# Kernel tuning notes

Hardware: AMD Instinct MI355X
Metric: run time of the kernel (lower is better)

## Reference

```python
import jax, jax.numpy as jnp
import numpy as np

B, C, L, H = 4, 128, 4096, 4
GROUPS, EPS = 32, 1e-5


def group_norm(x, gamma, beta):
    # x: [B, C, L]; normalize per (batch, group) over (C//G, L)
    b, c, l = x.shape
    xg = x.reshape(b, GROUPS, c // GROUPS, l)
    mu = jnp.mean(xg, axis=(2, 3), keepdims=True)
    var = jnp.var(xg, axis=(2, 3), keepdims=True)
    xn = ((xg - mu) * jax.lax.rsqrt(var + EPS)).reshape(b, c, l)
    return xn * gamma[None, :, None] + beta[None, :, None]


def setup_inputs() -> dict:
    key = jax.random.key(0)
    k1, k2, k3 = jax.random.split(key, 3)
    return {
        "x": jax.random.normal(k1, (B, C, L), dtype=jnp.float32),
        "w_qkv": jax.random.normal(k2, (3 * C, C), dtype=jnp.float32) * 0.02,
        "w_proj": jax.random.normal(k3, (C, C), dtype=jnp.float32) * 0.02,
        "b_proj": jnp.zeros((C,), dtype=jnp.float32),
        "gn_gamma": jnp.ones((C,), dtype=jnp.float32),
        "gn_beta": jnp.zeros((C,), dtype=jnp.float32),
    }


def reference(x, w_qkv, w_proj, b_proj, gn_gamma, gn_beta):
    b, c, l = x.shape
    hd = c // H
    h = group_norm(x, gn_gamma, gn_beta)
    # 1x1 conv == channel matmul: [B, 3C, L]
    qkv = jnp.einsum('oc,bcl->bol', w_qkv, h)
    # torch reshape(B*H, 3C/H, L).chunk(3, dim=1): per-head contiguous slices
    qkv = qkv.reshape(b, H, 3 * hd, l)
    q, k, v = qkv[:, :, :hd], qkv[:, :, hd:2 * hd], qkv[:, :, 2 * hd:]
    scale = 1.0 / np.sqrt(np.sqrt(hd)).astype(np.float32)
    attn = jnp.einsum('bhct,bhcs->bhts', q * scale, k * scale)
    attn = jax.nn.softmax(attn, axis=-1)
    o = jnp.einsum('bhts,bhcs->bhct', attn, v).reshape(b, c, l)
    o = jnp.einsum('oc,bcl->bol', w_proj, o) + b_proj[None, :, None]
    return o + x
```

## Files before the change

### kernel.cpp

```cpp
#include <hip/hip_runtime.h>
#include <hip/hip_bf16.h>
#include <cstdint>
#include <cstddef>


#define B_ 4
#define C_ 128
#define L_ 4096
#define H_ 4
#define HD_ 32
#define NG_ 32
#define CPG_ 4
#define EPS_ 1e-5f
#define QKSCALE_ 0.5050097650430367f

typedef __attribute__((ext_vector_type(8))) short bf16x8;
typedef __attribute__((ext_vector_type(8))) unsigned short u16x8;
typedef __attribute__((ext_vector_type(4))) float f32x4;
typedef __attribute__((ext_vector_type(2))) _Float16 f16x2;
typedef __attribute__((ext_vector_type(4))) _Float16 f16x4;

#if __has_builtin(__builtin_amdgcn_exp2f)
#define EXP2F(x) __builtin_amdgcn_exp2f(x)
#else
#define EXP2F(x) exp2f(x)
#endif

#if __has_builtin(__builtin_amdgcn_mfma_f32_16x16x16f16)
#define MFMA_PV(a, b, c) __builtin_amdgcn_mfma_f32_16x16x16f16((a), (b), (c), 0, 0, 0)
#elif __has_builtin(__builtin_amdgcn_mfma_f32_16x16x16_f16)
#define MFMA_PV(a, b, c) __builtin_amdgcn_mfma_f32_16x16x16_f16((a), (b), (c), 0, 0, 0)
#else
#define MFMA_PV(a, b, c) __builtin_amdgcn_mfma_f32_16x16x16f16((a), (b), (c), 0, 0, 0)
#endif

__device__ __forceinline__ float bu2f(unsigned short u) {
  return __builtin_bit_cast(float, (unsigned int)(((unsigned int)u) << 16));
}
__device__ __forceinline__ unsigned short f2bu(float f) {
  unsigned int u = __builtin_bit_cast(unsigned int, f);
  unsigned int r = (u + 0x7fffu + ((u >> 16) & 1u)) >> 16;
  return (unsigned short)r;
}
__device__ __forceinline__ float4 u42f4(ushort4 u) {
  return make_float4(bu2f(u.x), bu2f(u.y), bu2f(u.z), bu2f(u.w));
}
__device__ __forceinline__ unsigned int pkbf(float a, float b) {
  return (unsigned int)f2bu(a) | ((unsigned int)f2bu(b) << 16);
}
__device__ __forceinline__ f16x2 pkhf2(float a, float b) {
#if __has_builtin(__builtin_amdgcn_cvt_pkrtz)
  return __builtin_bit_cast(f16x2, __builtin_amdgcn_cvt_pkrtz(a, b));
#else
  f16x2 r;
  r[0] = (_Float16)a;
  r[1] = (_Float16)b;
  return r;
#endif
}
__device__ __forceinline__ unsigned int pkhf(float a, float b) {
  return __builtin_bit_cast(unsigned int, pkhf2(a, b));
}

__device__ __forceinline__ bool detect_fast(const ushort* x) {
  __shared__ int flag_s;
  int t = threadIdx.x;
  if (t < 64) {
    int e = (x[t] >> 7) & 0xFF;
    unsigned long long m = __ballot((e < 64) || (e > 192));
    if (t == 0) flag_s = (__popcll(m) > 4) ? 1 : 0;
  }
  __syncthreads();
  return flag_s != 0;
}

__device__ __forceinline__ float4 ldx4(const void* x, size_t idx, bool f32) {
  if (f32) return *((const float4*)x + (idx >> 2));
  ushort4 u = *((const ushort4*)x + (idx >> 2));
  return u42f4(u);
}

__global__ __launch_bounds__(512) void gn_fused(const void* __restrict__ x,
                                                const void* __restrict__ wq,
                                                const void* __restrict__ wp,
                                                const void* __restrict__ bp,
                                                const void* __restrict__ gm,
                                                const void* __restrict__ bt,
                                                ushort* __restrict__ wq_b,
                                                ushort* __restrict__ wp_b,
                                                float* __restrict__ bp_f,
                                                ushort* __restrict__ h_bf) {
  bool f32 = detect_fast((const ushort*)x);
  int blk = blockIdx.x;
  int t = threadIdx.x;

  if (blk >= 128) {
    int i0 = ((blk - 128) * 512 + t) * 4;
#pragma unroll
    for (int k = 0; k < 4; ++k) {
      int i = i0 + k;
      if (i >= 65664) break;
      if (i < 49152) {
        wq_b[i] = f32 ? f2bu(((const float*)wq)[i]) : ((const ushort*)wq)[i];
      } else if (i < 65536) {
        int off = i - 49152;
        wp_b[off] = f32 ? f2bu(((const float*)wp)[off]) : ((const ushort*)wp)[off];
      } else {
        int off = i - 65536;
        bp_f[off] = f32 ? ((const float*)bp)[off] : bu2f(((const ushort*)bp)[off]);
      }
    }
    return;
  }

  int b = blk >> 5, g = blk & 31;
  size_t base = ((size_t)b * C_ + (size_t)g * CPG_) * L_;

  float s = 0.f, ss = 0.f;
#pragma unroll
  for (int i = 0; i < 8; ++i) {
    size_t e = base + i * 2048 + t * 4;
    float4 f = ldx4(x, e, f32);
    s += f.x + f.y + f.z + f.w;
    ss += f.x * f.x + f.y * f.y + f.z * f.z + f.w * f.w;
  }
#pragma unroll
  for (int m = 32; m >= 1; m >>= 1) {
    s += __shfl_xor(s, m, 64);
    ss += __shfl_xor(ss, m, 64);
  }
  __shared__ float red[8][2];
  int wv = t >> 6;
  if ((t & 63) == 0) { red[wv][0] = s; red[wv][1] = ss; }
  __syncthreads();
  float ts = 0.f, tss = 0.f;
#pragma unroll
  for (int i = 0; i < 8; ++i) { ts += red[i][0]; tss += red[i][1]; }
  float mu = ts * (1.0f / 16384.0f);
  float var = tss * (1.0f / 16384.0f) - mu * mu;
  float rs = rsqrtf(var + EPS_);

  float a[CPG_], bb[CPG_];
#pragma unroll
  for (int c = 0; c < CPG_; ++c) {
    int gi = g * CPG_ + c;
    float ga = f32 ? ((const float*)gm)[gi] : bu2f(((const ushort*)gm)[gi]);
    float be = f32 ? ((const float*)bt)[gi] : bu2f(((const ushort*)bt)[gi]);
    a[c] = ga * rs;
    bb[c] = be - mu * ga * rs;
  }
#pragma unroll
  for (int i = 0; i < 8; ++i) {
    int e = i * 2048 + t * 4;
    int ch = e >> 12;
    float4 f = ldx4(x, base + e, f32);
    ushort4 o;
    o.x = f2bu(f.x * a[ch] + bb[ch]);
    o.y = f2bu(f.y * a[ch] + bb[ch]);
    o.z = f2bu(f.z * a[ch] + bb[ch]);
    o.w = f2bu(f.w * a[ch] + bb[ch]);
    *(ushort4*)(h_bf + base + e) = o;
  }
}

__global__ __launch_bounds__(256) void qkv_kernel(const ushort* __restrict__ wq_b,
                                                  const ushort* __restrict__ h_bf,
                                                  ushort* __restrict__ Qt,
                                                  ushort* __restrict__ Kt,
                                                  ushort* __restrict__ Vb) {
  __shared__ alignas(16) ushort Hs[64][136];
  __shared__ alignas(16) float Ls[64][69];

  int lx = blockIdx.x, oz = blockIdx.y, b = blockIdx.z;
  int t = threadIdx.x;
  int w = t >> 6, lane = t & 63, l16 = lane & 15, q = lane >> 4, q8 = q * 8;

  {
    int u = t & 63, lh = (t >> 6) * 16;
    const ushort* h0 = h_bf + ((size_t)b * C_ + 2 * u) * L_ + (size_t)lx * 64 + lh;
    u16x8 a0 = *(const u16x8*)h0;
    u16x8 a1 = *(const u16x8*)(h0 + 8);
    u16x8 b0 = *(const u16x8*)(h0 + L_);
    u16x8 b1 = *(const u16x8*)(h0 + L_ + 8);
#pragma unroll
    for (int j = 0; j < 8; ++j)
      *(unsigned int*)&Hs[lh + j][2 * u] = (unsigned int)a0[j] | ((unsigned int)b0[j] << 16);
#pragma unroll
    for (int j = 0; j < 8; ++j)
      *(unsigned int*)&Hs[lh + 8 + j][2 * u] = (unsigned int)a1[j] | ((unsigned int)b1[j] << 16);
  }
  __syncthreads();

  for (int j = 0; j < 2; ++j) {
    int oy = oz * 2 + j;
    const ushort* wg = wq_b + (size_t)(oy * 64 + w * 16 + l16) * C_;

    f32x4 acc[4] = {{0.f, 0.f, 0.f, 0.f}, {0.f, 0.f, 0.f, 0.f},
                    {0.f, 0.f, 0.f, 0.f}, {0.f, 0.f, 0.f, 0.f}};
#pragma unroll
    for (int kc = 0; kc < 4; ++kc) {
      bf16x8 aw = *(const bf16x8*)(wg + kc * 32 + q8);
#pragma unroll
      for (int nb = 0; nb < 4; ++nb) {
        bf16x8 bh = *(const bf16x8*)&Hs[nb * 16 + l16][kc * 32 + q8];
        acc[nb] = __builtin_amdgcn_mfma_f32_16x16x32_bf16(aw, bh, acc[nb], 0, 0, 0);
      }
    }
    __syncthreads();
#pragma unroll
    for (int nb = 0; nb < 4; ++nb)
#pragma unroll
      for (int r = 0; r < 4; ++r)
        Ls[nb * 16 + l16][w * 16 + 4 * q + r] = acc[nb][r];
    __syncthreads();

#pragma unroll
    for (int hhalf = 0; hhalf < 2; ++hhalf) {
      int hh = oy * 2 + hhalf;
      int type = hh % 3, head = hh / 3;
      size_t bh = (size_t)b * H_ + head;
      if (type == 2) {
        int c_loc = t >> 3, l8 = (t & 7) * 8;
        float v[8];
#pragma unroll
        for (int jj = 0; jj < 8; ++jj) v[jj] = Ls[l8 + jj][hhalf * 32 + c_loc];
        uint4 u;
        u.x = pkhf(v[0], v[1]);
        u.y = pkhf(v[2], v[3]);
        u.z = pkhf(v[4], v[5]);
        u.w = pkhf(v[6], v[7]);
        *(uint4*)(Vb + (bh * 32 + c_loc) * L_ + (size_t)lx * 64 + l8) = u;
      } else {
        ushort* dst = type ? Kt : Qt;
        int l = t >> 2, seg = (t & 3) * 8;
        const float* src = &Ls[l][hhalf * 32 + seg];
        uint4 u;
        u.x = pkbf(src[0] * QKSCALE_, src[1] * QKSCALE_);
        u.y = pkbf(src[2] * QKSCALE_, src[3] * QKSCALE_);
        u.z = pkbf(src[4] * QKSCALE_, src[5] * QKSCALE_);
        u.w = pkbf(src[6] * QKSCALE_, src[7] * QKSCALE_);
        *(uint4*)(dst + ((bh * L_) + lx * 64 + l) * 32 + seg) = u;
      }
    }
  }
}

__global__ __launch_bounds__(256) void attn_kernel(const ushort* __restrict__ Qt,
                                                   const ushort* __restrict__ Kt,
                                                   const ushort* __restrict__ Vb,
                                                   ushort* __restrict__ ot) {
  __shared__ alignas(16) ushort Ks[2][2048];
  __shared__ alignas(16) ushort Vs[2][32][72];

  int t = threadIdx.x;
  int w = t >> 6, lane = t & 63, l16 = lane & 15, q = lane >> 4;
  int tq0 = blockIdx.x * 64;
  int bh = blockIdx.y;
  int b = bh >> 2, head = bh & 3;
  const ushort* Qg = Qt + ((size_t)bh * L_ + tq0) * 32;
  const ushort* Kg = Kt + (size_t)bh * L_ * 32;
  const ushort* Vg = Vb + (size_t)bh * 32 * L_;

  int krow = (t & 15) | ((t >> 6) << 4);
  int kq8 = ((t >> 4) & 3) * 8;
  const ushort* kgp = Kg + (size_t)krow * 32 + kq8;
  int vc = t >> 3, vsl = (t & 7) * 8;
  const ushort* vgp = Vg + (size_t)vc * L_ + vsl;
  int trow = w * 16 + l16;
  int q8 = q * 8, q4 = q * 4;

  bf16x8 qfrag = *(const bf16x8*)(Qg + (size_t)trow * 32 + q8);

  *(uint4*)&Ks[0][t * 8] = *(const uint4*)kgp;
  *(uint4*)&Vs[0][vc][vsl] = *(const uint4*)vgp;
  __syncthreads();

  f32x4 accA = {0.f, 0.f, 0.f, 0.f};
  f32x4 accB = {0.f, 0.f, 0.f, 0.f};
  float lpart = 0.f;
  const ushort* kg_n = kgp + 2048;
  const ushort* vg_n = vgp + 64;
  const ushort* kf0 = &Ks[0][lane * 8];
  const ushort* kf1 = &Ks[1][lane * 8];

#pragma unroll 2
  for (int it = 0; it < 64; ++it) {
    int bc = it & 1;
    if (it < 63) {
      *(uint4*)&Ks[bc ^ 1][t * 8] = *(const uint4*)kg_n;
      *(uint4*)&Vs[bc ^ 1][vc][vsl] = *(const uint4*)vg_n;
      kg_n += 2048;
      vg_n += 64;
    }

    const ushort* kf = bc ? kf1 : kf0;
    f32x4 sf[4];
#pragma unroll
    for (int n = 0; n < 4; ++n) {
      bf16x8 ak = *(const bf16x8*)(kf + n * 512);
      f32x4 z = {0.f, 0.f, 0.f, 0.f};
      sf[n] = __builtin_amdgcn_mfma_f32_16x16x32_bf16(ak, qfrag, z, 0, 0, 0);
    }

#pragma unroll
    for (int n = 0; n < 4; ++n) {
      float p0 = EXP2F(sf[n][0]);
      float p1 = EXP2F(sf[n][1]);
      float p2 = EXP2F(sf[n][2]);
      float p3 = EXP2F(sf[n][3]);
      lpart += (p0 + p1) + (p2 + p3);
      f16x2 e01 = pkhf2(p0, p1);
      f16x2 e23 = pkhf2(p2, p3);
      f16x4 pb = __builtin_shufflevector(e01, e23, 0, 1, 2, 3);
      f16x4 va0 = *(const f16x4*)&Vs[bc][l16][n * 16 + q4];
      f16x4 va1 = *(const f16x4*)&Vs[bc][16 + l16][n * 16 + q4];
      accA = MFMA_PV(va0, pb, accA);
      accB = MFMA_PV(va1, pb, accB);
    }
    __syncthreads();
  }

  lpart += __shfl_xor(lpart, 16, 64);
  lpart += __shfl_xor(lpart, 32, 64);
  float inv = 1.0f / lpart;

  __syncthreads();
  ushort* Ep = &Ks[0][0];
#pragma unroll
  for (int r = 0; r < 2; ++r) {
    *(unsigned int*)&Ep[trow * 40 + q4 + 2 * r] =
        pkbf(accA[2 * r] * inv, accA[2 * r + 1] * inv);
    *(unsigned int*)&Ep[trow * 40 + 16 + q4 + 2 * r] =
        pkbf(accB[2 * r] * inv, accB[2 * r + 1] * inv);
  }
  __syncthreads();
  {
    int row = t >> 2, seg = (t & 3) * 8;
    *(uint4*)(ot + ((size_t)b * L_ + tq0 + row) * C_ + head * 32 + seg) =
        *(const uint4*)&Ep[row * 40 + seg];
  }
}

__global__ __launch_bounds__(256) void proj_kernel(const ushort* __restrict__ wp_b,
                                                   const float* __restrict__ bias,
                                                   const void* __restrict__ x,
                                                   const ushort* __restrict__ ot,
                                                   void* __restrict__ out) {
  bool f32 = detect_fast((const ushort*)x);
  __shared__ alignas(16) float Ls[64][37];

  int lx = blockIdx.x, oy = blockIdx.y, b = blockIdx.z;
  int t = threadIdx.x;
  int w = t >> 6, lane = t & 63, l16 = lane & 15, q = lane >> 4, q8 = q * 8;

  const ushort* wg = wp_b + (size_t)(oy * 64 + w * 16 + l16) * C_;
  const ushort* og = ot + ((size_t)b * L_ + (size_t)lx * 32) * C_;

  f32x4 acc[2] = {{0.f, 0.f, 0.f, 0.f}, {0.f, 0.f, 0.f, 0.f}};
#pragma unroll
  for (int kc = 0; kc < 4; ++kc) {
    bf16x8 aw = *(const bf16x8*)(wg + kc * 32 + q8);
#pragma unroll
    for (int nb = 0; nb < 2; ++nb) {
      bf16x8 bo = *(const bf16x8*)(og + (size_t)(nb * 16 + l16) * C_ + kc * 32 + q8);
      acc[nb] = __builtin_amdgcn_mfma_f32_16x16x32_bf16(aw, bo, acc[nb], 0, 0, 0);
    }
  }
#pragma unroll
  for (int nb = 0; nb < 2; ++nb)
#pragma unroll
    for (int r = 0; r < 4; ++r)
      Ls[w * 16 + 4 * q + r][nb * 16 + l16] = acc[nb][r];
  __syncthreads();

  {
    int o_loc = t >> 2, ls0 = (t & 3) * 8;
    float bv = bias[oy * 64 + o_loc];
    size_t off = ((size_t)b * C_ + oy * 64 + o_loc) * L_ + (size_t)lx * 32 + ls0;
#pragma unroll
    for (int jj = 0; jj < 2; ++jj) {
      float4 xf = ldx4(x, off + jj * 4, f32);
      const float* sp = &Ls[o_loc][ls0 + jj * 4];
      float4 r = make_float4(sp[0] + bv + xf.x, sp[1] + bv + xf.y,
                             sp[2] + bv + xf.z, sp[3] + bv + xf.w);
      if (f32) {
        *(float4*)((float*)out + off + jj * 4) = r;
      } else {
        *(ushort4*)((ushort*)out + off + jj * 4) =
            make_ushort4(f2bu(r.x), f2bu(r.y), f2bu(r.z), f2bu(r.w));
      }
    }
  }
}

extern "C" void kernel_launch(void* const* d_in, const int* in_sizes, int n_in,
                              void* d_out, int out_size, void* d_ws, size_t ws_size,
                              hipStream_t stream) {
  const void* x      = d_in[0];
  const void* w_qkv  = d_in[1];
  const void* w_proj = d_in[2];
  const void* b_proj = d_in[3];
  const void* gamma  = d_in[4];
  const void* beta   = d_in[5];

  char* wsb = (char*)d_ws;
  ushort* wq_b = (ushort*)(wsb + 0);
  ushort* wp_b = (ushort*)(wsb + 98304);
  float* bp_f  = (float*)(wsb + 131072);
  ushort* h_bf = (ushort*)(wsb + 1048576);
  ushort* Qt   = (ushort*)(wsb + 8388608);
  ushort* Kt   = (ushort*)(wsb + 12582912);
  ushort* Vb   = (ushort*)(wsb + 16777216);
  ushort* ot   = (ushort*)(wsb + 20971520);

  gn_fused<<<dim3(161), dim3(512), 0, stream>>>(x, w_qkv, w_proj, b_proj, gamma, beta,
                                                wq_b, wp_b, bp_f, h_bf);
  qkv_kernel<<<dim3(L_ / 64, 3, B_), dim3(256), 0, stream>>>(wq_b, h_bf, Qt, Kt, Vb);
  attn_kernel<<<dim3(L_ / 64, B_ * H_), dim3(256), 0, stream>>>(Qt, Kt, Vb, ot);
  proj_kernel<<<dim3(L_ / 32, C_ / 64, B_), dim3(256), 0, stream>>>(wp_b, bp_f, x, ot, d_out);
}
```

Before: 158.8 us.

## Fold GroupNorm apply into QKV load and widen attention KV tile

The GroupNorm kernel now only computes per-channel scale/shift pairs, and the QKV kernel reads x directly and applies the normalization while staging to shared memory. This removes the write and re-read of the bf16 normalized activation buffer. The attention kernel also processes 128 keys per iteration instead of 64, halving loop iterations and barriers at the cost of doubled shared memory per block. The QKV kernel reads x three times (once per output group), and in fp32 that means more bytes per load than the old bf16 buffer, and the larger LDS footprint may lower attention occupancy.

```diff
diff --git a/kernel.cpp b/kernel.cpp
--- a/kernel.cpp
+++ b/kernel.cpp
@@ -28,8 +28,6 @@
 
 #if __has_builtin(__builtin_amdgcn_mfma_f32_16x16x16f16)
 #define MFMA_PV(a, b, c) __builtin_amdgcn_mfma_f32_16x16x16f16((a), (b), (c), 0, 0, 0)
-#elif __has_builtin(__builtin_amdgcn_mfma_f32_16x16x16_f16)
-#define MFMA_PV(a, b, c) __builtin_amdgcn_mfma_f32_16x16x16_f16((a), (b), (c), 0, 0, 0)
 #else
 #define MFMA_PV(a, b, c) __builtin_amdgcn_mfma_f32_16x16x16f16((a), (b), (c), 0, 0, 0)
 #endif
@@ -80,7 +78,7 @@
   return u42f4(u);
 }
 
-__global__ __launch_bounds__(512) void gn_fused(const void* __restrict__ x,
+__global__ __launch_bounds__(256) void gn_stats(const void* __restrict__ x,
                                                 const void* __restrict__ wq,
                                                 const void* __restrict__ wp,
                                                 const void* __restrict__ bp,
@@ -89,15 +87,15 @@
                                                 ushort* __restrict__ wq_b,
                                                 ushort* __restrict__ wp_b,
                                                 float* __restrict__ bp_f,
-                                                ushort* __restrict__ h_bf) {
+                                                float2* __restrict__ gn_ab) {
   bool f32 = detect_fast((const ushort*)x);
   int blk = blockIdx.x;
   int t = threadIdx.x;
 
   if (blk >= 128) {
-    int i0 = ((blk - 128) * 512 + t) * 4;
-#pragma unroll
-    for (int k = 0; k < 4; ++k) {
+    int i0 = ((blk - 128) * 256 + t) * 8;
+#pragma unroll
+    for (int k = 0; k < 8; ++k) {
       int i = i0 + k;
       if (i >= 65664) break;
       if (i < 49152) {
@@ -118,8 +116,8 @@
 
   float s = 0.f, ss = 0.f;
 #pragma unroll
-  for (int i = 0; i < 8; ++i) {
-    size_t e = base + i * 2048 + t * 4;
+  for (int i = 0; i < 16; ++i) {
+    size_t e = base + i * 1024 + t * 4;
     float4 f = ldx4(x, e, f32);
     s += f.x + f.y + f.z + f.w;
     ss += f.x * f.x + f.y * f.y + f.z * f.z + f.w * f.w;
@@ -129,45 +127,31 @@
     s += __shfl_xor(s, m, 64);
     ss += __shfl_xor(ss, m, 64);
   }
-  __shared__ float red[8][2];
+  __shared__ float red[4][2];
   int wv = t >> 6;
   if ((t & 63) == 0) { red[wv][0] = s; red[wv][1] = ss; }
   __syncthreads();
-  float ts = 0.f, tss = 0.f;
-#pragma unroll
-  for (int i = 0; i < 8; ++i) { ts += red[i][0]; tss += red[i][1]; }
+  float ts = red[0][0] + red[1][0] + red[2][0] + red[3][0];
+  float tss = red[0][1] + red[1][1] + red[2][1] + red[3][1];
   float mu = ts * (1.0f / 16384.0f);
   float var = tss * (1.0f / 16384.0f) - mu * mu;
   float rs = rsqrtf(var + EPS_);
 
-  float a[CPG_], bb[CPG_];
-#pragma unroll
-  for (int c = 0; c < CPG_; ++c) {
-    int gi = g * CPG_ + c;
+  if (t < CPG_) {
+    int gi = g * CPG_ + t;
     float ga = f32 ? ((const float*)gm)[gi] : bu2f(((const ushort*)gm)[gi]);
     float be = f32 ? ((const float*)bt)[gi] : bu2f(((const ushort*)bt)[gi]);
-    a[c] = ga * rs;
-    bb[c] = be - mu * ga * rs;
-  }
-#pragma unroll
-  for (int i = 0; i < 8; ++i) {
-    int e = i * 2048 + t * 4;
-    int ch = e >> 12;
-    float4 f = ldx4(x, base + e, f32);
-    ushort4 o;
-    o.x = f2bu(f.x * a[ch] + bb[ch]);
-    o.y = f2bu(f.y * a[ch] + bb[ch]);
-    o.z = f2bu(f.z * a[ch] + bb[ch]);
-    o.w = f2bu(f.w * a[ch] + bb[ch]);
-    *(ushort4*)(h_bf + base + e) = o;
+    gn_ab[b * C_ + gi] = make_float2(ga * rs, be - mu * ga * rs);
   }
 }
 
 __global__ __launch_bounds__(256) void qkv_kernel(const ushort* __restrict__ wq_b,
-                                                  const ushort* __restrict__ h_bf,
+                                                  const void* __restrict__ x,
+                                                  const float2* __restrict__ gn_ab,
                                                   ushort* __restrict__ Qt,
                                                   ushort* __restrict__ Kt,
                                                   ushort* __restrict__ Vb) {
+  bool f32 = detect_fast((const ushort*)x);
   __shared__ alignas(16) ushort Hs[64][136];
   __shared__ alignas(16) float Ls[64][69];
 
@@ -177,17 +161,22 @@
 
   {
     int u = t & 63, lh = (t >> 6) * 16;
-    const ushort* h0 = h_bf + ((size_t)b * C_ + 2 * u) * L_ + (size_t)lx * 64 + lh;
-    u16x8 a0 = *(const u16x8*)h0;
-    u16x8 a1 = *(const u16x8*)(h0 + 8);
-    u16x8 b0 = *(const u16x8*)(h0 + L_);
-    u16x8 b1 = *(const u16x8*)(h0 + L_ + 8);
-#pragma unroll
-    for (int j = 0; j < 8; ++j)
-      *(unsigned int*)&Hs[lh + j][2 * u] = (unsigned int)a0[j] | ((unsigned int)b0[j] << 16);
-#pragma unroll
-    for (int j = 0; j < 8; ++j)
-      *(unsigned int*)&Hs[lh + 8 + j][2 * u] = (unsigned int)a1[j] | ((unsigned int)b1[j] << 16);
+    int c0 = 2 * u;
+    float2 ab0 = gn_ab[b * C_ + c0];
+    float2 ab1 = gn_ab[b * C_ + c0 + 1];
+    size_t xo = ((size_t)b * C_ + c0) * L_ + (size_t)lx * 64 + lh;
+#pragma unroll
+    for (int j = 0; j < 4; ++j) {
+      float4 f0 = ldx4(x, xo + j * 4, f32);
+      float4 f1 = ldx4(x, xo + L_ + j * 4, f32);
+      float n0[4] = {f0.x * ab0.x + ab0.y, f0.y * ab0.x + ab0.y,
+                     f0.z * ab0.x + ab0.y, f0.w * ab0.x + ab0.y};
+      float n1[4] = {f1.x * ab1.x + ab1.y, f1.y * ab1.x + ab1.y,
+                     f1.z * ab1.x + ab1.y, f1.w * ab1.x + ab1.y};
+#pragma unroll
+      for (int k = 0; k < 4; ++k)
+        *(unsigned int*)&Hs[lh + j * 4 + k][c0] = pkbf(n0[k], n1[k]);
+    }
   }
   __syncthreads();
 
@@ -249,8 +238,8 @@
                                                    const ushort* __restrict__ Kt,
                                                    const ushort* __restrict__ Vb,
                                                    ushort* __restrict__ ot) {
-  __shared__ alignas(16) ushort Ks[2][2048];
-  __shared__ alignas(16) ushort Vs[2][32][72];
+  __shared__ alignas(16) ushort Ks[2][4096];
+  __shared__ alignas(16) ushort Vs[2][32][136];
 
   int t = threadIdx.x;
   int w = t >> 6, lane = t & 63, l16 = lane & 15, q = lane >> 4;
@@ -272,50 +261,54 @@
   bf16x8 qfrag = *(const bf16x8*)(Qg + (size_t)trow * 32 + q8);
 
   *(uint4*)&Ks[0][t * 8] = *(const uint4*)kgp;
+  *(uint4*)&Ks[0][2048 + t * 8] = *(const uint4*)(kgp + 2048);
   *(uint4*)&Vs[0][vc][vsl] = *(const uint4*)vgp;
+  *(uint4*)&Vs[0][vc][64 + vsl] = *(const uint4*)(vgp + 64);
   __syncthreads();
 
   f32x4 accA = {0.f, 0.f, 0.f, 0.f};
   f32x4 accB = {0.f, 0.f, 0.f, 0.f};
   float lpart = 0.f;
-  const ushort* kg_n = kgp + 2048;
-  const ushort* vg_n = vgp + 64;
-  const ushort* kf0 = &Ks[0][lane * 8];
-  const ushort* kf1 = &Ks[1][lane * 8];
+  const ushort* kg_n = kgp + 4096;
+  const ushort* vg_n = vgp + 128;
 
 #pragma unroll 2
-  for (int it = 0; it < 64; ++it) {
+  for (int it = 0; it < 32; ++it) {
     int bc = it & 1;
-    if (it < 63) {
+    if (it < 31) {
       *(uint4*)&Ks[bc ^ 1][t * 8] = *(const uint4*)kg_n;
+      *(uint4*)&Ks[bc ^ 1][2048 + t * 8] = *(const uint4*)(kg_n + 2048);
       *(uint4*)&Vs[bc ^ 1][vc][vsl] = *(const uint4*)vg_n;
-      kg_n += 2048;
-      vg_n += 64;
-    }
-
-    const ushort* kf = bc ? kf1 : kf0;
-    f32x4 sf[4];
-#pragma unroll
-    for (int n = 0; n < 4; ++n) {
-      bf16x8 ak = *(const bf16x8*)(kf + n * 512);
-      f32x4 z = {0.f, 0.f, 0.f, 0.f};
-      sf[n] = __builtin_amdgcn_mfma_f32_16x16x32_bf16(ak, qfrag, z, 0, 0, 0);
-    }
-
-#pragma unroll
-    for (int n = 0; n < 4; ++n) {
-      float p0 = EXP2F(sf[n][0]);
-      float p1 = EXP2F(sf[n][1]);
-      float p2 = EXP2F(sf[n][2]);
-      float p3 = EXP2F(sf[n][3]);
-      lpart += (p0 + p1) + (p2 + p3);
-      f16x2 e01 = pkhf2(p0, p1);
-      f16x2 e23 = pkhf2(p2, p3);
-      f16x4 pb = __builtin_shufflevector(e01, e23, 0, 1, 2, 3);
-      f16x4 va0 = *(const f16x4*)&Vs[bc][l16][n * 16 + q4];
-      f16x4 va1 = *(const f16x4*)&Vs[bc][16 + l16][n * 16 + q4];
-      accA = MFMA_PV(va0, pb, accA);
-      accB = MFMA_PV(va1, pb, accB);
+      *(uint4*)&Vs[bc ^ 1][vc][64 + vsl] = *(const uint4*)(vg_n + 64);
+      kg_n += 4096;
+      vg_n += 128;
+    }
+
+#pragma unroll
+    for (int hh2 = 0; hh2 < 2; ++hh2) {
+      const ushort* kf = &Ks[bc][hh2 * 2048 + lane * 8];
+      f32x4 sf[4];
+#pragma unroll
+      for (int n = 0; n < 4; ++n) {
+        bf16x8 ak = *(const bf16x8*)(kf + n * 512);
+        f32x4 z = {0.f, 0.f, 0.f, 0.f};
+        sf[n] = __builtin_amdgcn_mfma_f32_16x16x32_bf16(ak, qfrag, z, 0, 0, 0);
+      }
+#pragma unroll
+      for (int n = 0; n < 4; ++n) {
+        float p0 = EXP2F(sf[n][0]);
+        float p1 = EXP2F(sf[n][1]);
+        float p2 = EXP2F(sf[n][2]);
+        float p3 = EXP2F(sf[n][3]);
+        lpart += (p0 + p1) + (p2 + p3);
+        f16x2 e01 = pkhf2(p0, p1);
+        f16x2 e23 = pkhf2(p2, p3);
+        f16x4 pb = __builtin_shufflevector(e01, e23, 0, 1, 2, 3);
+        f16x4 va0 = *(const f16x4*)&Vs[bc][l16][hh2 * 64 + n * 16 + q4];
+        f16x4 va1 = *(const f16x4*)&Vs[bc][16 + l16][hh2 * 64 + n * 16 + q4];
+        accA = MFMA_PV(va0, pb, accA);
+        accB = MFMA_PV(va1, pb, accB);
+      }
     }
     __syncthreads();
   }
@@ -404,18 +397,18 @@
   const void* beta   = d_in[5];
 
   char* wsb = (char*)d_ws;
-  ushort* wq_b = (ushort*)(wsb + 0);
-  ushort* wp_b = (ushort*)(wsb + 98304);
-  float* bp_f  = (float*)(wsb + 131072);
-  ushort* h_bf = (ushort*)(wsb + 1048576);
-  ushort* Qt   = (ushort*)(wsb + 8388608);
-  ushort* Kt   = (ushort*)(wsb + 12582912);
-  ushort* Vb   = (ushort*)(wsb + 16777216);
-  ushort* ot   = (ushort*)(wsb + 20971520);
-
-  gn_fused<<<dim3(161), dim3(512), 0, stream>>>(x, w_qkv, w_proj, b_proj, gamma, beta,
-                                                wq_b, wp_b, bp_f, h_bf);
-  qkv_kernel<<<dim3(L_ / 64, 3, B_), dim3(256), 0, stream>>>(wq_b, h_bf, Qt, Kt, Vb);
+  ushort* wq_b  = (ushort*)(wsb + 0);
+  ushort* wp_b  = (ushort*)(wsb + 98304);
+  float*  bp_f  = (float*)(wsb + 131072);
+  float2* gn_ab = (float2*)(wsb + 131584);
+  ushort* Qt    = (ushort*)(wsb + 8388608);
+  ushort* Kt    = (ushort*)(wsb + 12582912);
+  ushort* Vb    = (ushort*)(wsb + 16777216);
+  ushort* ot    = (ushort*)(wsb + 20971520);
+
+  gn_stats<<<dim3(161), dim3(256), 0, stream>>>(x, w_qkv, w_proj, b_proj, gamma, beta,
+                                                wq_b, wp_b, bp_f, gn_ab);
+  qkv_kernel<<<dim3(L_ / 64, 3, B_), dim3(256), 0, stream>>>(wq_b, x, gn_ab, Qt, Kt, Vb);
   attn_kernel<<<dim3(L_ / 64, B_ * H_), dim3(256), 0, stream>>>(Qt, Kt, Vb, ot);
   proj_kernel<<<dim3(L_ / 32, C_ / 64, B_), dim3(256), 0, stream>>>(wp_b, bp_f, x, ot, d_out);
 }
```

Result: faster. 152.5 us (-4.0%).
